# Performance work log

Measured on AMD Instinct MI355X. Metric: run time of the kernel, lower is better.

Reference implementation:

```python
import jax, jax.numpy as jnp
import numpy as np

D = 256
NHEAD = 4
T = 8
TOTAL_STEPS = 64
EPS = 1e-5


def _ln(x, g, b):
    m = jnp.mean(x, -1, keepdims=True)
    v = jnp.mean((x - m) ** 2, -1, keepdims=True)
    return (x - m) / jnp.sqrt(v + EPS) * g + b


def setup_inputs() -> dict:
    key = jax.random.key(0)
    ks = iter(jax.random.split(key, 64))

    def W(shape):
        return jax.random.normal(next(ks), shape, jnp.float32) * 0.02

    B = 1024
    inp = {
        "fen_tokens": jax.random.randint(next(ks), (B, 77), 0, 128, jnp.int32),
        "uci_token": jax.random.randint(next(ks), (B, 1), 0, 1968, jnp.int32),
        "fen_emb_w": W((128, D)),
        "uci_emb_w": W((1968, D)),
        "pos_emb_w": W((78, D)),
        "tl_wqkv": W((4, D, 3 * D)), "tl_bqkv": jnp.zeros((4, 3 * D)),
        "tl_wo": W((4, D, D)), "tl_bo": jnp.zeros((4, D)),
        "tl_ln1_g": jnp.ones((4, D)), "tl_ln1_b": jnp.zeros((4, D)),
        "tl_w1": W((4, D, 2048)), "tl_b1": jnp.zeros((4, 2048)),
        "tl_w2": W((4, 2048, D)), "tl_b2": jnp.zeros((4, D)),
        "tl_ln2_g": jnp.ones((4, D)), "tl_ln2_b": jnp.zeros((4, D)),
        "post_ln_g": jnp.ones(D), "post_ln_b": jnp.zeros(D),
        "pool_w1": W((D, D)), "pool_b1": jnp.zeros(D),
        "pool_w2": W((D, D)), "pool_b2": jnp.zeros(D),
        "L_w1": W((3 * D, D)), "L_b1": jnp.zeros(D),
        "L_w2": W((D, D)), "L_b2": jnp.zeros(D),
        "L_ln_g": jnp.ones(D), "L_ln_b": jnp.zeros(D),
        "H_w1": W((2 * D, D)), "H_b1": jnp.zeros(D),
        "H_w2": W((D, D)), "H_b2": jnp.zeros(D),
        "H_ln_g": jnp.ones(D), "H_ln_b": jnp.zeros(D),
        "vh_ln_g": jnp.ones(D), "vh_ln_b": jnp.zeros(D),
        "vh_w1": W((D, D)), "vh_b1": jnp.zeros(D),
        "vh_w2": W((D, 128)), "vh_b2": jnp.zeros(128),
    }
    return inp


def _forward(fen_tokens, uci_token, fen_emb_w, uci_emb_w, pos_emb_w,
             tl_wqkv, tl_bqkv, tl_wo, tl_bo, tl_ln1_g, tl_ln1_b,
             tl_w1, tl_b1, tl_w2, tl_b2, tl_ln2_g, tl_ln2_b,
             post_ln_g, post_ln_b, pool_w1, pool_b1, pool_w2, pool_b2,
             L_w1, L_b1, L_w2, L_b2, L_ln_g, L_ln_b,
             H_w1, H_b1, H_w2, H_b2, H_ln_g, H_ln_b,
             vh_ln_g, vh_ln_b, vh_w1, vh_b1, vh_w2, vh_b2):
    B = fen_tokens.shape[0]
    hd = D // NHEAD
    # embed: [B,77,D] cat [B,1,D] -> [B,78,D], plus positional embedding
    x = jnp.concatenate([fen_emb_w[fen_tokens], uci_emb_w[uci_token[:, 0]][:, None, :]], axis=1)
    x = x + pos_emb_w[None]
    # 4-layer post-norm transformer encoder (relu FFN, d_ff=2048)
    for l in range(4):
        qkv = x @ tl_wqkv[l] + tl_bqkv[l]
        q, k, v = jnp.split(qkv, 3, axis=-1)
        q = q.reshape(B, -1, NHEAD, hd).transpose(0, 2, 1, 3)
        k = k.reshape(B, -1, NHEAD, hd).transpose(0, 2, 1, 3)
        v = v.reshape(B, -1, NHEAD, hd).transpose(0, 2, 1, 3)
        att = jax.nn.softmax(jnp.einsum('bhqd,bhkd->bhqk', q, k) / jnp.sqrt(jnp.float32(hd)), axis=-1)
        o = jnp.einsum('bhqk,bhkd->bhqd', att, v).transpose(0, 2, 1, 3).reshape(B, -1, D)
        x = _ln(x + o @ tl_wo[l] + tl_bo[l], tl_ln1_g[l], tl_ln1_b[l])
        ff = jax.nn.relu(x @ tl_w1[l] + tl_b1[l]) @ tl_w2[l] + tl_b2[l]
        x = _ln(x + ff, tl_ln2_g[l], tl_ln2_b[l])
    x = _ln(x, post_ln_g, post_ln_b)
    pooled = jax.nn.relu(jax.nn.relu(x @ pool_w1 + pool_b1) @ pool_w2 + pool_b2)
    out = pooled.mean(axis=1)  # [B,D]

    def l_net(t):
        return _ln(jax.nn.relu(jax.nn.relu(t @ L_w1 + L_b1) @ L_w2 + L_b2), L_ln_g, L_ln_b)

    def h_net(t):
        return _ln(jax.nn.relu(jax.nn.relu(t @ H_w1 + H_b1) @ H_w2 + H_b2), H_ln_g, H_ln_b)

    z0 = jnp.zeros((B, D), x.dtype)

    def step(carry, i):
        zL, zH = carry
        zL = l_net(jnp.concatenate([zL, zH, out], axis=-1))
        zH_new = h_net(jnp.concatenate([zH, zL], axis=-1))
        zH = jnp.where(((i + 1) % T) == 0, zH_new, zH)
        return (zL, zH), None

    # first 63 steps run under torch.no_grad -> stop_gradient on the scan result
    (zL, zH), _ = jax.lax.scan(step, (z0, z0), jnp.arange(TOTAL_STEPS - 1))
    zL = jax.lax.stop_gradient(zL)
    zH = jax.lax.stop_gradient(zH)
    zL = l_net(jnp.concatenate([zL, zH, out], axis=-1))
    zH = h_net(jnp.concatenate([zH, zL], axis=-1))
    vh = _ln(zH, vh_ln_g, vh_ln_b)
    return jax.nn.relu(vh @ vh_w1 + vh_b1) @ vh_w2 + vh_b2  # [B, num_bins]


def reference(fen_tokens, uci_token, fen_emb_w, uci_emb_w, pos_emb_w,
              tl_wqkv, tl_bqkv, tl_wo, tl_bo, tl_ln1_g, tl_ln1_b,
              tl_w1, tl_b1, tl_w2, tl_b2, tl_ln2_g, tl_ln2_b,
              post_ln_g, post_ln_b, pool_w1, pool_b1, pool_w2, pool_b2,
              L_w1, L_b1, L_w2, L_b2, L_ln_g, L_ln_b,
              H_w1, H_b1, H_w2, H_b2, H_ln_g, H_ln_b,
              vh_ln_g, vh_ln_b, vh_w1, vh_b1, vh_w2, vh_b2):
    return _forward(fen_tokens, uci_token, fen_emb_w, uci_emb_w, pos_emb_w,
                    tl_wqkv, tl_bqkv, tl_wo, tl_bo, tl_ln1_g, tl_ln1_b,
                    tl_w1, tl_b1, tl_w2, tl_b2, tl_ln2_g, tl_ln2_b,
                    post_ln_g, post_ln_b, pool_w1, pool_b1, pool_w2, pool_b2,
                    L_w1, L_b1, L_w2, L_b2, L_ln_g, L_ln_b,
                    H_w1, H_b1, H_w2, H_b2, H_ln_g, H_ln_b,
                    vh_ln_g, vh_ln_b, vh_w1, vh_b1, vh_w2, vh_b2)
```

## Files before the change

kernel.cpp:

```cpp
#include <hip/hip_runtime.h>
#include <cstdint>
#include <cstddef>

typedef unsigned short u16;
typedef short s8v __attribute__((ext_vector_type(8)));
typedef float f32x4 __attribute__((ext_vector_type(4)));
typedef u16 u16x4 __attribute__((ext_vector_type(4)));

#define DEV __device__ __forceinline__

DEV u16 f2bf(float f) {
  union { float f; uint32_t u; } a; a.f = f;
  uint32_t u = a.u;
  return (u16)((u + 0x7fffu + ((u >> 16) & 1u)) >> 16);
}
DEV float bf2f(u16 h) {
  union { uint32_t u; float f; } a; a.u = ((uint32_t)h) << 16;
  return a.f;
}
DEV void f2bf_split(float v, u16& hi, u16& lo) {
  hi = f2bf(v);
  lo = f2bf(v - bf2f(hi));
}

__global__ __launch_bounds__(256) void k_transpose(const float* __restrict__ W,
                                                   u16* __restrict__ WThi,
                                                   u16* __restrict__ WTlo, int K, int N) {
  __shared__ float tile[32][33];
  int k0 = blockIdx.x * 32, n0 = blockIdx.y * 32;
  int tx = threadIdx.x & 31, ty = threadIdx.x >> 5;
#pragma unroll
  for (int i = 0; i < 32; i += 8)
    tile[ty + i][tx] = W[(size_t)(k0 + ty + i) * N + n0 + tx];
  __syncthreads();
#pragma unroll
  for (int i = 0; i < 32; i += 8) {
    float w = tile[tx][ty + i];
    u16 hi, lo; f2bf_split(w, hi, lo);
    size_t idx = (size_t)(n0 + ty + i) * K + k0 + tx;
    WThi[idx] = hi;
    WTlo[idx] = lo;
  }
}

__global__ __launch_bounds__(256) void k_embed(const int* __restrict__ fen,
                                               const int* __restrict__ uci,
                                               const float* __restrict__ femb,
                                               const float* __restrict__ uemb,
                                               const float* __restrict__ pemb,
                                               float* __restrict__ xf,
                                               u16* __restrict__ xhi, u16* __restrict__ xlo,
                                               int b0) {
  int row = blockIdx.x;
  int c = threadIdx.x;
  int bl = row / 78, p = row % 78;
  int b = b0 + bl;
  int tok;
  const float* e;
  if (p < 77) { tok = fen[b * 77 + p]; e = femb; }
  else        { tok = uci[b];          e = uemb; }
  float v = e[(size_t)tok * 256 + c] + pemb[p * 256 + c];
  size_t idx = (size_t)row * 256 + c;
  xf[idx] = v;
  u16 hi, lo; f2bf_split(v, hi, lo);
  xhi[idx] = hi;
  xlo[idx] = lo;
}

template <bool RELU, bool OUT_F32, bool OUT_SPLIT>
__global__ __launch_bounds__(256) void k_gemm(const u16* __restrict__ Ahi,
                                              const u16* __restrict__ Alo,
                                              const u16* __restrict__ Bhi,
                                              const u16* __restrict__ Blo,
                                              const float* __restrict__ bias,
                                              float* __restrict__ Cf,
                                              u16* __restrict__ Chi, u16* __restrict__ Clo,
                                              int M, int N, int K) {
  __shared__ __align__(16) u16 Ah[128][40];
  __shared__ __align__(16) u16 Al[128][40];
  __shared__ __align__(16) u16 Bh[128][40];
  __shared__ __align__(16) u16 Bl[128][40];
  const int tid = threadIdx.x;
  const int wid = tid >> 6, lane = tid & 63;
  const int wr = wid >> 1, wc = wid & 1;
  const int m0 = blockIdx.x * 128, n0 = blockIdx.y * 128;
  f32x4 acc[4][4] = {};
  const int sr = tid >> 2;
  const int sc = (tid & 3) * 8;

  for (int kt = 0; kt < K; kt += 32) {
#pragma unroll
    for (int i = 0; i < 2; i++) {
      int row = sr + i * 64;
      size_t ga = (size_t)(m0 + row) * K + kt + sc;
      size_t gb = (size_t)(n0 + row) * K + kt + sc;
      *(s8v*)&Ah[row][sc] = *(const s8v*)&Ahi[ga];
      *(s8v*)&Al[row][sc] = *(const s8v*)&Alo[ga];
      *(s8v*)&Bh[row][sc] = *(const s8v*)&Bhi[gb];
      *(s8v*)&Bl[row][sc] = *(const s8v*)&Blo[gb];
    }
    __syncthreads();
    const int fr = lane & 15, fc = (lane >> 4) * 8;
    s8v bh[4], bl[4];
#pragma unroll
    for (int j = 0; j < 4; j++) {
      bh[j] = *(const s8v*)&Bh[wc * 64 + j * 16 + fr][fc];
      bl[j] = *(const s8v*)&Bl[wc * 64 + j * 16 + fr][fc];
    }
#pragma unroll
    for (int i = 0; i < 4; i++) {
      s8v ah = *(const s8v*)&Ah[wr * 64 + i * 16 + fr][fc];
      s8v al = *(const s8v*)&Al[wr * 64 + i * 16 + fr][fc];
#pragma unroll
      for (int j = 0; j < 4; j++) {
        acc[i][j] = __builtin_amdgcn_mfma_f32_16x16x32_bf16(ah, bh[j], acc[i][j], 0, 0, 0);
        acc[i][j] = __builtin_amdgcn_mfma_f32_16x16x32_bf16(ah, bl[j], acc[i][j], 0, 0, 0);
        acc[i][j] = __builtin_amdgcn_mfma_f32_16x16x32_bf16(al, bh[j], acc[i][j], 0, 0, 0);
      }
    }
    __syncthreads();
  }
#pragma unroll
  for (int j = 0; j < 4; j++) {
    int col = n0 + wc * 64 + j * 16 + (lane & 15);
    float bv = bias[col];
#pragma unroll
    for (int i = 0; i < 4; i++) {
#pragma unroll
      for (int r = 0; r < 4; r++) {
        int row = m0 + wr * 64 + i * 16 + (lane >> 4) * 4 + r;
        float v = acc[i][j][r] + bv;
        if (RELU) v = fmaxf(v, 0.f);
        size_t idx = (size_t)row * N + col;
        if (OUT_F32) Cf[idx] = v;
        if (OUT_SPLIT) {
          u16 hi, lo; f2bf_split(v, hi, lo);
          Chi[idx] = hi;
          Clo[idx] = lo;
        }
      }
    }
  }
}

__global__ __launch_bounds__(128) void k_attn(const float* __restrict__ qkvf,
                                              u16* __restrict__ ohi, u16* __restrict__ olo) {
  __shared__ float Ks[78][68];
  __shared__ float Vs[78][68];
  __shared__ float Ss[78][79];
  const int bl = blockIdx.x >> 2, h = blockIdx.x & 3;
  const int tid = threadIdx.x;
  const size_t rowbase = (size_t)bl * 78;
  for (int ci = tid; ci < 1248; ci += 128) {
    int row = ci >> 4, c4 = (ci & 15) * 4;
    const float* kp = &qkvf[(rowbase + row) * 768 + 256 + h * 64 + c4];
    *(float4*)&Ks[row][c4] = *(const float4*)kp;
    *(float4*)&Vs[row][c4] = *(const float4*)(kp + 256);
  }
  __syncthreads();
  const int q = tid;
  if (q < 78) {
    float qv[64];
    const float* qp = &qkvf[(rowbase + q) * 768 + h * 64];
#pragma unroll
    for (int d4 = 0; d4 < 64; d4 += 4) {
      float4 t = *(const float4*)&qp[d4];
      qv[d4] = t.x; qv[d4 + 1] = t.y; qv[d4 + 2] = t.z; qv[d4 + 3] = t.w;
    }
    float mx = -1e30f;
    for (int k = 0; k < 78; k++) {
      float s = 0.f;
#pragma unroll
      for (int d = 0; d < 64; d++) s += qv[d] * Ks[k][d];
      s *= 0.125f;
      Ss[q][k] = s;
      mx = fmaxf(mx, s);
    }
    float sum = 0.f;
    for (int k = 0; k < 78; k++) { float e = __expf(Ss[q][k] - mx); Ss[q][k] = e; sum += e; }
    float inv = 1.f / sum;
    float ov[64];
#pragma unroll
    for (int d = 0; d < 64; d++) ov[d] = 0.f;
    for (int k = 0; k < 78; k++) {
      float p = Ss[q][k];
#pragma unroll
      for (int d = 0; d < 64; d++) ov[d] += p * Vs[k][d];
    }
    size_t obase = (rowbase + q) * 256 + h * 64;
#pragma unroll
    for (int d8 = 0; d8 < 64; d8 += 8) {
      s8v whi, wlo;
#pragma unroll
      for (int j = 0; j < 8; j++) {
        u16 hi, lo; f2bf_split(ov[d8 + j] * inv, hi, lo);
        whi[j] = (short)hi; wlo[j] = (short)lo;
      }
      *(s8v*)&ohi[obase + d8] = whi;
      *(s8v*)&olo[obase + d8] = wlo;
    }
  }
}

template <bool ADD>
__global__ __launch_bounds__(256) void k_addln(const float* __restrict__ x,
                                               const float* __restrict__ t,
                                               const float* __restrict__ g,
                                               const float* __restrict__ b,
                                               float* __restrict__ xo,
                                               u16* __restrict__ xhi, u16* __restrict__ xlo) {
  int row = blockIdx.x * 4 + (threadIdx.x >> 6);
  int lane = threadIdx.x & 63;
  const float* xr = x + (size_t)row * 256;
  float4 v = *(const float4*)&xr[lane * 4];
  if (ADD) {
    float4 tv = *(const float4*)&t[(size_t)row * 256 + lane * 4];
    v.x += tv.x; v.y += tv.y; v.z += tv.z; v.w += tv.w;
  }
  float s = v.x + v.y + v.z + v.w;
  float q = v.x * v.x + v.y * v.y + v.z * v.z + v.w * v.w;
#pragma unroll
  for (int off = 32; off; off >>= 1) { s += __shfl_down(s, off); q += __shfl_down(q, off); }
  s = __shfl(s, 0); q = __shfl(q, 0);
  float mean = s * (1.f / 256.f);
  float var = q * (1.f / 256.f) - mean * mean;
  float rstd = rsqrtf(var + 1e-5f);
  float4 gg = *(const float4*)&g[lane * 4];
  float4 bb = *(const float4*)&b[lane * 4];
  float o0 = (v.x - mean) * rstd * gg.x + bb.x;
  float o1 = (v.y - mean) * rstd * gg.y + bb.y;
  float o2 = (v.z - mean) * rstd * gg.z + bb.z;
  float o3 = (v.w - mean) * rstd * gg.w + bb.w;
  size_t base = (size_t)row * 256 + lane * 4;
  *(float4*)&xo[base] = make_float4(o0, o1, o2, o3);
  u16 h0, l0, h1, l1, h2, l2, h3, l3;
  f2bf_split(o0, h0, l0); f2bf_split(o1, h1, l1);
  f2bf_split(o2, h2, l2); f2bf_split(o3, h3, l3);
  u16x4 vh = { h0, h1, h2, h3 };
  u16x4 vl = { l0, l1, l2, l3 };
  *(u16x4*)&xhi[base] = vh;
  *(u16x4*)&xlo[base] = vl;
}

__global__ __launch_bounds__(256) void k_mean(const float* __restrict__ p2,
                                              float* __restrict__ out, int b0) {
  int bl = blockIdx.x, d = threadIdx.x;
  const float* base = p2 + (size_t)bl * 78 * 256 + d;
  float s = 0.f;
#pragma unroll 13
  for (int p = 0; p < 78; p++) s += base[(size_t)p * 256];
  out[(size_t)(b0 + bl) * 256 + d] = s * (1.f / 78.f);
}

__global__ __launch_bounds__(256) void k_zero(float* p, int n) {
  int i = blockIdx.x * 256 + threadIdx.x;
  if (i < n) p[i] = 0.f;
}

__global__ __launch_bounds__(256) void k_lbase(const float* __restrict__ zH,
                                               const float* __restrict__ out,
                                               const float* __restrict__ W1,
                                               const float* __restrict__ b1,
                                               float* __restrict__ baseL) {
  int r0 = blockIdx.x * 4, col = threadIdx.x;
  __shared__ float t[4][512];
#pragma unroll
  for (int i = 0; i < 4; i++) {
    t[i][col] = zH[(size_t)(r0 + i) * 256 + col];
    t[i][256 + col] = out[(size_t)(r0 + i) * 256 + col];
  }
  __syncthreads();
  float acc[4];
#pragma unroll
  for (int i = 0; i < 4; i++) acc[i] = b1[col];
  for (int k = 0; k < 512; k++) {
    float w = W1[(size_t)(256 + k) * 256 + col];
#pragma unroll
    for (int i = 0; i < 4; i++) acc[i] += t[i][k] * w;
  }
#pragma unroll
  for (int i = 0; i < 4; i++) baseL[(size_t)(r0 + i) * 256 + col] = acc[i];
}

DEV void row_ln_stats(float a2[4], int col, float (*redS)[4], float (*redQ)[4],
                      float mean[4], float rstd[4]) {
  int wid = col >> 6, lane = col & 63;
#pragma unroll
  for (int i = 0; i < 4; i++) {
    float s = a2[i], q = a2[i] * a2[i];
#pragma unroll
    for (int off = 32; off; off >>= 1) { s += __shfl_down(s, off); q += __shfl_down(q, off); }
    if (lane == 0) { redS[i][wid] = s; redQ[i][wid] = q; }
  }
  __syncthreads();
#pragma unroll
  for (int i = 0; i < 4; i++) {
    float s = redS[i][0] + redS[i][1] + redS[i][2] + redS[i][3];
    float q = redQ[i][0] + redQ[i][1] + redQ[i][2] + redQ[i][3];
    mean[i] = s * (1.f / 256.f);
    float var = q * (1.f / 256.f) - mean[i] * mean[i];
    rstd[i] = rsqrtf(var + 1e-5f);
  }
}

__global__ __launch_bounds__(256) void k_lstep(float* __restrict__ zL,
                                               const float* __restrict__ baseL,
                                               const float* __restrict__ W1,
                                               const float* __restrict__ W2,
                                               const float* __restrict__ b2,
                                               const float* __restrict__ g,
                                               const float* __restrict__ bb) {
  int r0 = blockIdx.x * 4, col = threadIdx.x;
  __shared__ float t[4][256];
  __shared__ float h1[4][256];
  __shared__ float redS[4][4], redQ[4][4];
#pragma unroll
  for (int i = 0; i < 4; i++) t[i][col] = zL[(size_t)(r0 + i) * 256 + col];
  __syncthreads();
  float acc[4];
#pragma unroll
  for (int i = 0; i < 4; i++) acc[i] = baseL[(size_t)(r0 + i) * 256 + col];
  for (int k = 0; k < 256; k++) {
    float w = W1[(size_t)k * 256 + col];
#pragma unroll
    for (int i = 0; i < 4; i++) acc[i] += t[i][k] * w;
  }
#pragma unroll
  for (int i = 0; i < 4; i++) h1[i][col] = fmaxf(acc[i], 0.f);
  __syncthreads();
  float a2[4];
#pragma unroll
  for (int i = 0; i < 4; i++) a2[i] = b2[col];
  for (int k = 0; k < 256; k++) {
    float w = W2[(size_t)k * 256 + col];
#pragma unroll
    for (int i = 0; i < 4; i++) a2[i] += h1[i][k] * w;
  }
#pragma unroll
  for (int i = 0; i < 4; i++) a2[i] = fmaxf(a2[i], 0.f);
  float mean[4], rstd[4];
  row_ln_stats(a2, col, redS, redQ, mean, rstd);
#pragma unroll
  for (int i = 0; i < 4; i++)
    zL[(size_t)(r0 + i) * 256 + col] = (a2[i] - mean[i]) * rstd[i] * g[col] + bb[col];
}

__global__ __launch_bounds__(256) void k_hstep(float* __restrict__ zH,
                                               const float* __restrict__ zL,
                                               const float* __restrict__ W1,
                                               const float* __restrict__ b1,
                                               const float* __restrict__ W2,
                                               const float* __restrict__ b2,
                                               const float* __restrict__ g,
                                               const float* __restrict__ bb) {
  int r0 = blockIdx.x * 4, col = threadIdx.x;
  __shared__ float t[4][512];
  __shared__ float h1[4][256];
  __shared__ float redS[4][4], redQ[4][4];
#pragma unroll
  for (int i = 0; i < 4; i++) {
    t[i][col] = zH[(size_t)(r0 + i) * 256 + col];
    t[i][256 + col] = zL[(size_t)(r0 + i) * 256 + col];
  }
  __syncthreads();
  float acc[4];
#pragma unroll
  for (int i = 0; i < 4; i++) acc[i] = b1[col];
  for (int k = 0; k < 512; k++) {
    float w = W1[(size_t)k * 256 + col];
#pragma unroll
    for (int i = 0; i < 4; i++) acc[i] += t[i][k] * w;
  }
#pragma unroll
  for (int i = 0; i < 4; i++) h1[i][col] = fmaxf(acc[i], 0.f);
  __syncthreads();
  float a2[4];
#pragma unroll
  for (int i = 0; i < 4; i++) a2[i] = b2[col];
  for (int k = 0; k < 256; k++) {
    float w = W2[(size_t)k * 256 + col];
#pragma unroll
    for (int i = 0; i < 4; i++) a2[i] += h1[i][k] * w;
  }
#pragma unroll
  for (int i = 0; i < 4; i++) a2[i] = fmaxf(a2[i], 0.f);
  float mean[4], rstd[4];
  row_ln_stats(a2, col, redS, redQ, mean, rstd);
#pragma unroll
  for (int i = 0; i < 4; i++)
    zH[(size_t)(r0 + i) * 256 + col] = (a2[i] - mean[i]) * rstd[i] * g[col] + bb[col];
}

__global__ __launch_bounds__(256) void k_vh(const float* __restrict__ zH,
                                            const float* __restrict__ g,
                                            const float* __restrict__ bb,
                                            const float* __restrict__ W1,
                                            const float* __restrict__ b1,
                                            const float* __restrict__ W2,
                                            const float* __restrict__ b2,
                                            float* __restrict__ out) {
  int r0 = blockIdx.x * 4, col = threadIdx.x;
  __shared__ float t[4][256];
  __shared__ float h1[4][256];
  __shared__ float redS[4][4], redQ[4][4];
  float v[4];
#pragma unroll
  for (int i = 0; i < 4; i++) v[i] = zH[(size_t)(r0 + i) * 256 + col];
  float mean[4], rstd[4];
  row_ln_stats(v, col, redS, redQ, mean, rstd);
#pragma unroll
  for (int i = 0; i < 4; i++) t[i][col] = (v[i] - mean[i]) * rstd[i] * g[col] + bb[col];
  __syncthreads();
  float acc[4];
#pragma unroll
  for (int i = 0; i < 4; i++) acc[i] = b1[col];
  for (int k = 0; k < 256; k++) {
    float w = W1[(size_t)k * 256 + col];
#pragma unroll
    for (int i = 0; i < 4; i++) acc[i] += t[i][k] * w;
  }
#pragma unroll
  for (int i = 0; i < 4; i++) h1[i][col] = fmaxf(acc[i], 0.f);
  __syncthreads();
  if (col < 128) {
    float a2[4];
#pragma unroll
    for (int i = 0; i < 4; i++) a2[i] = b2[col];
    for (int k = 0; k < 256; k++) {
      float w = W2[(size_t)k * 128 + col];
#pragma unroll
      for (int i = 0; i < 4; i++) a2[i] += h1[i][k] * w;
    }
#pragma unroll
    for (int i = 0; i < 4; i++) out[(size_t)(r0 + i) * 128 + col] = a2[i];
  }
}

extern "C" void kernel_launch(void* const* d_in, const int* in_sizes, int n_in,
                              void* d_out, int out_size, void* d_ws, size_t ws_size,
                              hipStream_t stream) {
  (void)in_sizes; (void)n_in; (void)out_size;
  const int* fen = (const int*)d_in[0];
  const int* uci = (const int*)d_in[1];
  const float* femb = (const float*)d_in[2];
  const float* uemb = (const float*)d_in[3];
  const float* pemb = (const float*)d_in[4];
  const float* wqkv = (const float*)d_in[5];
  const float* bqkv = (const float*)d_in[6];
  const float* wo_ = (const float*)d_in[7];
  const float* bo_ = (const float*)d_in[8];
  const float* ln1g = (const float*)d_in[9];
  const float* ln1b = (const float*)d_in[10];
  const float* w1_ = (const float*)d_in[11];
  const float* b1_ = (const float*)d_in[12];
  const float* w2_ = (const float*)d_in[13];
  const float* b2_ = (const float*)d_in[14];
  const float* ln2g = (const float*)d_in[15];
  const float* ln2b = (const float*)d_in[16];
  const float* postg = (const float*)d_in[17];
  const float* postb = (const float*)d_in[18];
  const float* pw1 = (const float*)d_in[19];
  const float* pb1 = (const float*)d_in[20];
  const float* pw2 = (const float*)d_in[21];
  const float* pb2 = (const float*)d_in[22];
  const float* Lw1 = (const float*)d_in[23];
  const float* Lb1 = (const float*)d_in[24];
  const float* Lw2 = (const float*)d_in[25];
  const float* Lb2 = (const float*)d_in[26];
  const float* Llng = (const float*)d_in[27];
  const float* Llnb = (const float*)d_in[28];
  const float* Hw1 = (const float*)d_in[29];
  const float* Hb1 = (const float*)d_in[30];
  const float* Hw2 = (const float*)d_in[31];
  const float* Hb2 = (const float*)d_in[32];
  const float* Hlng = (const float*)d_in[33];
  const float* Hlnb = (const float*)d_in[34];
  const float* vhg = (const float*)d_in[35];
  const float* vhb = (const float*)d_in[36];
  const float* vw1 = (const float*)d_in[37];
  const float* vb1 = (const float*)d_in[38];
  const float* vw2 = (const float*)d_in[39];
  const float* vb2 = (const float*)d_in[40];

  char* p = (char*)d_ws;
  auto alloc = [&](size_t bytes) -> void* {
    void* r = (void*)p;
    p += (bytes + 255) & ~(size_t)255;
    return r;
  };
  float* outf = (float*)alloc(1024 * 256 * 4);
  float* baseL = (float*)alloc(1024 * 256 * 4);
  float* zLH = (float*)alloc(2 * 1024 * 256 * 4);
  float* zL = zLH;
  float* zH = zLH + 1024 * 256;
  u16* wqThi = (u16*)alloc((size_t)4 * 768 * 256 * 2);
  u16* wqTlo = (u16*)alloc((size_t)4 * 768 * 256 * 2);
  u16* woThi = (u16*)alloc((size_t)4 * 256 * 256 * 2);
  u16* woTlo = (u16*)alloc((size_t)4 * 256 * 256 * 2);
  u16* w1Thi = (u16*)alloc((size_t)4 * 2048 * 256 * 2);
  u16* w1Tlo = (u16*)alloc((size_t)4 * 2048 * 256 * 2);
  u16* w2Thi = (u16*)alloc((size_t)4 * 256 * 2048 * 2);
  u16* w2Tlo = (u16*)alloc((size_t)4 * 256 * 2048 * 2);
  u16* pw1Thi = (u16*)alloc((size_t)256 * 256 * 2);
  u16* pw1Tlo = (u16*)alloc((size_t)256 * 256 * 2);
  u16* pw2Thi = (u16*)alloc((size_t)256 * 256 * 2);
  u16* pw2Tlo = (u16*)alloc((size_t)256 * 256 * 2);

  size_t fixed = (size_t)(p - (char*)d_ws);
  int NC = 16;
  for (int c : {8, 16, 4, 2, 1}) {
    size_t Mc_ = (size_t)(1024 / c) * 78;
    if (fixed + Mc_ * 15360 + (size_t)(1 << 20) <= ws_size) { NC = c; break; }
  }
  const int Bc = 1024 / NC;
  const size_t Mc = (size_t)Bc * 78;

  float* xf = (float*)alloc(Mc * 256 * 4);
  float* tmp = (float*)alloc(Mc * 256 * 4);
  u16* xhi = (u16*)alloc(Mc * 256 * 2);
  u16* xlo = (u16*)alloc(Mc * 256 * 2);
  float* qkvf = (float*)alloc(Mc * 768 * 4);
  u16* ohi = (u16*)alloc(Mc * 256 * 2);
  u16* olo = (u16*)alloc(Mc * 256 * 2);
  u16* hhi = (u16*)alloc(Mc * 2048 * 2);
  u16* hlo = (u16*)alloc(Mc * 2048 * 2);

  auto tr = [&](const float* W, u16* WThi, u16* WTlo, int K, int N) {
    k_transpose<<<dim3(K / 32, N / 32), 256, 0, stream>>>(W, WThi, WTlo, K, N);
  };
  for (int l = 0; l < 4; l++) {
    tr(wqkv + (size_t)l * 256 * 768, wqThi + (size_t)l * 768 * 256,
       wqTlo + (size_t)l * 768 * 256, 256, 768);
    tr(wo_ + (size_t)l * 256 * 256, woThi + (size_t)l * 256 * 256,
       woTlo + (size_t)l * 256 * 256, 256, 256);
    tr(w1_ + (size_t)l * 256 * 2048, w1Thi + (size_t)l * 2048 * 256,
       w1Tlo + (size_t)l * 2048 * 256, 256, 2048);
    tr(w2_ + (size_t)l * 2048 * 256, w2Thi + (size_t)l * 256 * 2048,
       w2Tlo + (size_t)l * 256 * 2048, 2048, 256);
  }
  tr(pw1, pw1Thi, pw1Tlo, 256, 256);
  tr(pw2, pw2Thi, pw2Tlo, 256, 256);

  const int MT = (int)(Mc / 128);
  for (int ch = 0; ch < NC; ch++) {
    int b0 = ch * Bc;
    k_embed<<<(int)Mc, 256, 0, stream>>>(fen, uci, femb, uemb, pemb, xf, xhi, xlo, b0);
    for (int l = 0; l < 4; l++) {
      k_gemm<false, true, false><<<dim3(MT, 6), 256, 0, stream>>>(
          xhi, xlo, wqThi + (size_t)l * 768 * 256, wqTlo + (size_t)l * 768 * 256,
          bqkv + l * 768, qkvf, nullptr, nullptr, (int)Mc, 768, 256);
      k_attn<<<Bc * 4, 128, 0, stream>>>(qkvf, ohi, olo);
      k_gemm<false, true, false><<<dim3(MT, 2), 256, 0, stream>>>(
          ohi, olo, woThi + (size_t)l * 256 * 256, woTlo + (size_t)l * 256 * 256,
          bo_ + l * 256, tmp, nullptr, nullptr, (int)Mc, 256, 256);
      k_addln<true><<<(int)(Mc / 4), 256, 0, stream>>>(
          xf, tmp, ln1g + l * 256, ln1b + l * 256, xf, xhi, xlo);
      k_gemm<true, false, true><<<dim3(MT, 16), 256, 0, stream>>>(
          xhi, xlo, w1Thi + (size_t)l * 2048 * 256, w1Tlo + (size_t)l * 2048 * 256,
          b1_ + l * 2048, nullptr, hhi, hlo, (int)Mc, 2048, 256);
      k_gemm<false, true, false><<<dim3(MT, 2), 256, 0, stream>>>(
          hhi, hlo, w2Thi + (size_t)l * 256 * 2048, w2Tlo + (size_t)l * 256 * 2048,
          b2_ + l * 256, tmp, nullptr, nullptr, (int)Mc, 256, 2048);
      k_addln<true><<<(int)(Mc / 4), 256, 0, stream>>>(
          xf, tmp, ln2g + l * 256, ln2b + l * 256, xf, xhi, xlo);
    }
    k_addln<false><<<(int)(Mc / 4), 256, 0, stream>>>(xf, nullptr, postg, postb, xf, xhi, xlo);
    k_gemm<true, false, true><<<dim3(MT, 2), 256, 0, stream>>>(
        xhi, xlo, pw1Thi, pw1Tlo, pb1, nullptr, ohi, olo, (int)Mc, 256, 256);
    k_gemm<true, true, false><<<dim3(MT, 2), 256, 0, stream>>>(
        ohi, olo, pw2Thi, pw2Tlo, pb2, tmp, nullptr, nullptr, (int)Mc, 256, 256);
    k_mean<<<Bc, 256, 0, stream>>>(tmp, outf, b0);
  }

  k_zero<<<(2 * 1024 * 256) / 256, 256, 0, stream>>>(zLH, 2 * 1024 * 256);
  for (int st = 0; st < 64; st++) {
    if ((st & 7) == 0)
      k_lbase<<<256, 256, 0, stream>>>(zH, outf, Lw1, Lb1, baseL);
    k_lstep<<<256, 256, 0, stream>>>(zL, baseL, Lw1, Lw2, Lb2, Llng, Llnb);
    if ((st & 7) == 7)
      k_hstep<<<256, 256, 0, stream>>>(zH, zL, Hw1, Hb1, Hw2, Hb2, Hlng, Hlnb);
  }
  k_vh<<<256, 256, 0, stream>>>(zH, vhg, vhb, vw1, vb1, vw2, vb2, (float*)d_out);
}
```

Baseline: 10.05 ms.

## Stage GEMM tiles via direct global-to-LDS loads with XOR swizzle

Replaces the register-staged global-to-shared copies in the split-bf16 GEMM with direct global_load_lds transfers. Each wave now fills one of the four tiles (A hi, A lo, B hi, B lo). The padded shared layout is replaced by an unpadded one with an XOR column swizzle to avoid bank conflicts on the fragment reads. It also changes the preferred chunk count to 4, giving fewer and larger batch chunks. The aim is to cut VGPR round trips and load instructions, at the cost of relying on the swizzle pattern being correct and on the larger workspace fitting.

```diff
diff --git a/kernel.cpp b/kernel.cpp
--- a/kernel.cpp
+++ b/kernel.cpp
@@ -8,6 +8,13 @@
 typedef u16 u16x4 __attribute__((ext_vector_type(4)));
 
 #define DEV __device__ __forceinline__
+
+typedef __attribute__((address_space(1))) const void* as1_cvp;
+typedef __attribute__((address_space(3))) void* as3_vp;
+
+DEV void gload_lds16(const u16* g, u16* l) {
+  __builtin_amdgcn_global_load_lds((as1_cvp)(const void*)g, (as3_vp)(void*)l, 16, 0, 0);
+}
 
 DEV u16 f2bf(float f) {
   union { float f; uint32_t u; } a; a.f = f;
@@ -76,41 +83,47 @@
                                               float* __restrict__ Cf,
                                               u16* __restrict__ Chi, u16* __restrict__ Clo,
                                               int M, int N, int K) {
-  __shared__ __align__(16) u16 Ah[128][40];
-  __shared__ __align__(16) u16 Al[128][40];
-  __shared__ __align__(16) u16 Bh[128][40];
-  __shared__ __align__(16) u16 Bl[128][40];
+  __shared__ __align__(16) u16 Ah[128][32];
+  __shared__ __align__(16) u16 Al[128][32];
+  __shared__ __align__(16) u16 Bh[128][32];
+  __shared__ __align__(16) u16 Bl[128][32];
   const int tid = threadIdx.x;
   const int wid = tid >> 6, lane = tid & 63;
   const int wr = wid >> 1, wc = wid & 1;
   const int m0 = blockIdx.x * 128, n0 = blockIdx.y * 128;
   f32x4 acc[4][4] = {};
-  const int sr = tid >> 2;
-  const int sc = (tid & 3) * 8;
+
+  const u16* gsel;
+  int rowbase;
+  if (wid == 0)      { gsel = Ahi; rowbase = m0; }
+  else if (wid == 1) { gsel = Alo; rowbase = m0; }
+  else if (wid == 2) { gsel = Bhi; rowbase = n0; }
+  else               { gsel = Blo; rowbase = n0; }
+  u16* lsel = (wid == 0) ? &Ah[0][0] : (wid == 1) ? &Al[0][0]
+            : (wid == 2) ? &Bh[0][0] : &Bl[0][0];
+  const int lrow = lane >> 2;
+  const int gcolo = (((lane & 3) ^ ((lane >> 2) & 3)) << 3);
+  const u16* gptr = gsel + (size_t)(rowbase + lrow) * K + gcolo;
+
+  const int fr = lane & 15;
+  const int rc = (((lane >> 4) ^ (lane & 3)) << 3);
 
   for (int kt = 0; kt < K; kt += 32) {
 #pragma unroll
-    for (int i = 0; i < 2; i++) {
-      int row = sr + i * 64;
-      size_t ga = (size_t)(m0 + row) * K + kt + sc;
-      size_t gb = (size_t)(n0 + row) * K + kt + sc;
-      *(s8v*)&Ah[row][sc] = *(const s8v*)&Ahi[ga];
-      *(s8v*)&Al[row][sc] = *(const s8v*)&Alo[ga];
-      *(s8v*)&Bh[row][sc] = *(const s8v*)&Bhi[gb];
-      *(s8v*)&Bl[row][sc] = *(const s8v*)&Blo[gb];
-    }
+    for (int c = 0; c < 8; c++)
+      gload_lds16(gptr + (size_t)(c * 16) * K, lsel + c * 16 * 32);
+    gptr += 32;
     __syncthreads();
-    const int fr = lane & 15, fc = (lane >> 4) * 8;
     s8v bh[4], bl[4];
 #pragma unroll
     for (int j = 0; j < 4; j++) {
-      bh[j] = *(const s8v*)&Bh[wc * 64 + j * 16 + fr][fc];
-      bl[j] = *(const s8v*)&Bl[wc * 64 + j * 16 + fr][fc];
+      bh[j] = *(const s8v*)&Bh[wc * 64 + j * 16 + fr][rc];
+      bl[j] = *(const s8v*)&Bl[wc * 64 + j * 16 + fr][rc];
     }
 #pragma unroll
     for (int i = 0; i < 4; i++) {
-      s8v ah = *(const s8v*)&Ah[wr * 64 + i * 16 + fr][fc];
-      s8v al = *(const s8v*)&Al[wr * 64 + i * 16 + fr][fc];
+      s8v ah = *(const s8v*)&Ah[wr * 64 + i * 16 + fr][rc];
+      s8v al = *(const s8v*)&Al[wr * 64 + i * 16 + fr][rc];
 #pragma unroll
       for (int j = 0; j < 4; j++) {
         acc[i][j] = __builtin_amdgcn_mfma_f32_16x16x32_bf16(ah, bh[j], acc[i][j], 0, 0, 0);
@@ -508,7 +521,7 @@
 
   size_t fixed = (size_t)(p - (char*)d_ws);
   int NC = 16;
-  for (int c : {8, 16, 4, 2, 1}) {
+  for (int c : {4, 8, 16, 2, 1}) {
     size_t Mc_ = (size_t)(1024 / c) * 78;
     if (fixed + Mc_ * 15360 + (size_t)(1 << 20) <= ws_size) { NC = c; break; }
   }
```

Measured after the change: 10.13 ms. About the same (+0.8%).
